# Optimization experiments

Measured on AMD Instinct MI355X. Metric: run time of the kernel, lower is better.

Reference implementation:

```python
import jax, jax.numpy as jnp
import numpy as np


def setup_inputs() -> dict:
    key = jax.random.key(0)
    k1, k2, k3 = jax.random.split(key, 3)
    H, W = 4096, 4096
    KH, KW = 3, 3
    return {
        "input": jax.random.normal(k1, (H, W), dtype=jnp.float32),
        "weight": jax.random.normal(k2, (KH, KW), dtype=jnp.float32),
        "bias": jax.random.normal(k3, (1,), dtype=jnp.float32),
    }


def reference(input, weight, bias):
    # VALID 2D cross-correlation of a single-channel image with a single kernel,
    # identical math to the original scalar double-loop: Y[i,j] = sum(X[i:i+h, j:j+w] * K) + b.
    x = input[None, None, :, :]   # NCHW, N=C=1
    k = weight[None, None, :, :]  # OIHW, O=I=1
    y = jax.lax.conv_general_dilated(
        x, k,
        window_strides=(1, 1),
        padding="VALID",
        dimension_numbers=("NCHW", "OIHW", "NCHW"),
    )[0, 0]  # [H-kh+1, W-kw+1]
    return y + bias[0]
```

## Files before the change

### kernel.cpp

```cpp
#include <hip/hip_runtime.h>

#define IW 4096
#define IH 4096
#define OH 4094
#define OW 4094
#define CG 1024
#define NWG 4096
#define XCHUNK 512

typedef float f32x4 __attribute__((ext_vector_type(4)));
typedef float f32x2 __attribute__((ext_vector_type(2)));

__global__ __launch_bounds__(256) void conv3x3_r4p(
    const float* __restrict__ in, const float* __restrict__ wgt,
    const float* __restrict__ bias, float* __restrict__ out) {

    int b   = blockIdx.x;
    int swz = (b & 7) * XCHUNK + (b >> 3);
    int idx = swz * 256 + (int)threadIdx.x;

    int cg   = idx & (CG - 1);
    int rg   = idx >> 10;
    int x    = cg << 2;
    int row0 = rg << 2;

    float wv[9];
#pragma unroll
    for (int i = 0; i < 9; ++i) wv[i] = wgt[i];
    float bs = bias[0];

    int nr    = (row0 + 4 <= OH) ? 4 : (OH - row0);
    int nload = nr + 2;

    float r[6][6];
#pragma unroll
    for (int t = 0; t < 6; ++t) {
        if (t < nload) {
            const float* rp = in + (size_t)(row0 + t) * IW + x;
            float4 a = *reinterpret_cast<const float4*>(rp);
            r[t][0] = a.x; r[t][1] = a.y; r[t][2] = a.z; r[t][3] = a.w;
            if (x + 5 < IW) {
                float2 e = *reinterpret_cast<const float2*>(rp + 4);
                r[t][4] = e.x; r[t][5] = e.y;
            } else { r[t][4] = 0.f; r[t][5] = 0.f; }
        } else {
#pragma unroll
            for (int j = 0; j < 6; ++j) r[t][j] = 0.f;
        }
    }

    float acc[4][4];
#pragma unroll
    for (int i = 0; i < 4; ++i)
#pragma unroll
        for (int c = 0; c < 4; ++c) acc[i][c] = bs;

#pragma unroll
    for (int orow = 0; orow < 4; ++orow) {
#pragma unroll
        for (int kh = 0; kh < 3; ++kh) {
            int t = orow + kh;
            float w0 = wv[kh * 3 + 0], w1 = wv[kh * 3 + 1], w2 = wv[kh * 3 + 2];
#pragma unroll
            for (int c = 0; c < 4; ++c)
                acc[orow][c] += w0 * r[t][c] + w1 * r[t][c + 1] + w2 * r[t][c + 2];
        }
    }

    int nc = (x + 4 <= OW) ? 4 : (OW - x);
#pragma unroll
    for (int orow = 0; orow < 4; ++orow) {
        if (orow < nr) {
            float* op = out + (size_t)(row0 + orow) * OW + x;
            if (nc == 4) {
                if ((orow & 1) == 0) {
                    *reinterpret_cast<f32x4*>(op) =
                        f32x4{ acc[orow][0], acc[orow][1], acc[orow][2], acc[orow][3] };
                } else {
                    *reinterpret_cast<f32x2*>(op)     = f32x2{ acc[orow][0], acc[orow][1] };
                    *reinterpret_cast<f32x2*>(op + 2) = f32x2{ acc[orow][2], acc[orow][3] };
                }
            } else {
                *reinterpret_cast<f32x2*>(op) = f32x2{ acc[orow][0], acc[orow][1] };
            }
        }
    }
}

extern "C" void kernel_launch(void* const* d_in, const int* in_sizes, int n_in,
                              void* d_out, int out_size, void* d_ws, size_t ws_size,
                              hipStream_t stream) {
    const float* in   = (const float*)d_in[0];
    const float* wgt  = (const float*)d_in[1];
    const float* bias = (const float*)d_in[2];
    float* out        = (float*)d_out;

    conv3x3_r4p<<<NWG, 256, 0, stream>>>(in, wgt, bias, out);
}
```

Before: 29.76 us.

## Compute two column tiles per thread and use nontemporal output stores

Result: slower. 30.96 us (+4.0%).

```diff
diff --git a/kernel.cpp b/kernel.cpp
--- a/kernel.cpp
+++ b/kernel.cpp
@@ -1,28 +1,30 @@
 #include <hip/hip_runtime.h>
 
 #define IW 4096
-#define IH 4096
 #define OH 4094
 #define OW 4094
-#define CG 1024
-#define NWG 4096
-#define XCHUNK 512
+#define NWG 2048
+#define XCHUNK 256
 
 typedef float f32x4 __attribute__((ext_vector_type(4)));
 typedef float f32x2 __attribute__((ext_vector_type(2)));
 
-__global__ __launch_bounds__(256) void conv3x3_r4p(
+__global__ __launch_bounds__(256) void conv3x3_dual(
     const float* __restrict__ in, const float* __restrict__ wgt,
     const float* __restrict__ bias, float* __restrict__ out) {
 
-    int b   = blockIdx.x;
-    int swz = (b & 7) * XCHUNK + (b >> 3);
-    int idx = swz * 256 + (int)threadIdx.x;
+    int b    = blockIdx.x;
+    int swz  = (b & 7) * XCHUNK + (b >> 3);
+    int lane = (int)threadIdx.x & 63;
+    int wib  = (int)threadIdx.x >> 6;
 
-    int cg   = idx & (CG - 1);
-    int rg   = idx >> 10;
-    int x    = cg << 2;
+    int wid  = swz * 4 + wib;
+    int wc   = wid & 7;
+    int rg   = wid >> 3;
     int row0 = rg << 2;
+
+    int x0 = wc * 512 + lane * 4;
+    int x1 = x0 + 256;
 
     float wv[9];
 #pragma unroll
@@ -32,56 +34,76 @@
     int nr    = (row0 + 4 <= OH) ? 4 : (OH - row0);
     int nload = nr + 2;
 
-    float r[6][6];
+    float r0[6][6], r1[6][6];
 #pragma unroll
     for (int t = 0; t < 6; ++t) {
         if (t < nload) {
-            const float* rp = in + (size_t)(row0 + t) * IW + x;
-            float4 a = *reinterpret_cast<const float4*>(rp);
-            r[t][0] = a.x; r[t][1] = a.y; r[t][2] = a.z; r[t][3] = a.w;
-            if (x + 5 < IW) {
-                float2 e = *reinterpret_cast<const float2*>(rp + 4);
-                r[t][4] = e.x; r[t][5] = e.y;
-            } else { r[t][4] = 0.f; r[t][5] = 0.f; }
+            const float* rp = in + (size_t)(row0 + t) * IW;
+            f32x4 a0 = *reinterpret_cast<const f32x4*>(rp + x0);
+            f32x4 a1 = *reinterpret_cast<const f32x4*>(rp + x1);
+            f32x2 e0 = *reinterpret_cast<const f32x2*>(rp + x0 + 4);
+            float e1a = 0.f, e1b = 0.f;
+            if (x1 + 5 < IW) {
+                f32x2 e1 = *reinterpret_cast<const f32x2*>(rp + x1 + 4);
+                e1a = e1[0]; e1b = e1[1];
+            }
+            r0[t][0]=a0[0]; r0[t][1]=a0[1]; r0[t][2]=a0[2]; r0[t][3]=a0[3];
+            r0[t][4]=e0[0]; r0[t][5]=e0[1];
+            r1[t][0]=a1[0]; r1[t][1]=a1[1]; r1[t][2]=a1[2]; r1[t][3]=a1[3];
+            r1[t][4]=e1a;   r1[t][5]=e1b;
         } else {
 #pragma unroll
-            for (int j = 0; j < 6; ++j) r[t][j] = 0.f;
+            for (int j = 0; j < 6; ++j) { r0[t][j] = 0.f; r1[t][j] = 0.f; }
         }
     }
 
-    float acc[4][4];
+    float acc0[4][4], acc1[4][4];
 #pragma unroll
     for (int i = 0; i < 4; ++i)
 #pragma unroll
-        for (int c = 0; c < 4; ++c) acc[i][c] = bs;
+        for (int c = 0; c < 4; ++c) { acc0[i][c] = bs; acc1[i][c] = bs; }
 
 #pragma unroll
     for (int orow = 0; orow < 4; ++orow) {
 #pragma unroll
         for (int kh = 0; kh < 3; ++kh) {
             int t = orow + kh;
-            float w0 = wv[kh * 3 + 0], w1 = wv[kh * 3 + 1], w2 = wv[kh * 3 + 2];
+            float w0 = wv[kh*3+0], w1 = wv[kh*3+1], w2 = wv[kh*3+2];
 #pragma unroll
-            for (int c = 0; c < 4; ++c)
-                acc[orow][c] += w0 * r[t][c] + w1 * r[t][c + 1] + w2 * r[t][c + 2];
+            for (int c = 0; c < 4; ++c) {
+                acc0[orow][c] += w0*r0[t][c] + w1*r0[t][c+1] + w2*r0[t][c+2];
+                acc1[orow][c] += w0*r1[t][c] + w1*r1[t][c+1] + w2*r1[t][c+2];
+            }
         }
     }
 
-    int nc = (x + 4 <= OW) ? 4 : (OW - x);
+    int nc1 = (x1 + 4 <= OW) ? 4 : (OW - x1);
 #pragma unroll
     for (int orow = 0; orow < 4; ++orow) {
         if (orow < nr) {
-            float* op = out + (size_t)(row0 + orow) * OW + x;
-            if (nc == 4) {
-                if ((orow & 1) == 0) {
-                    *reinterpret_cast<f32x4*>(op) =
-                        f32x4{ acc[orow][0], acc[orow][1], acc[orow][2], acc[orow][3] };
+            float* op0 = out + (size_t)(row0 + orow) * OW + x0;
+            float* op1 = out + (size_t)(row0 + orow) * OW + x1;
+            if ((orow & 1) == 0) {
+                f32x4 v = { acc0[orow][0], acc0[orow][1], acc0[orow][2], acc0[orow][3] };
+                __builtin_nontemporal_store(v, reinterpret_cast<f32x4*>(op0));
+                if (nc1 == 4) {
+                    f32x4 u = { acc1[orow][0], acc1[orow][1], acc1[orow][2], acc1[orow][3] };
+                    __builtin_nontemporal_store(u, reinterpret_cast<f32x4*>(op1));
                 } else {
-                    *reinterpret_cast<f32x2*>(op)     = f32x2{ acc[orow][0], acc[orow][1] };
-                    *reinterpret_cast<f32x2*>(op + 2) = f32x2{ acc[orow][2], acc[orow][3] };
+                    f32x2 u = { acc1[orow][0], acc1[orow][1] };
+                    __builtin_nontemporal_store(u, reinterpret_cast<f32x2*>(op1));
                 }
             } else {
-                *reinterpret_cast<f32x2*>(op) = f32x2{ acc[orow][0], acc[orow][1] };
+                f32x2 v0 = { acc0[orow][0], acc0[orow][1] };
+                f32x2 v1 = { acc0[orow][2], acc0[orow][3] };
+                __builtin_nontemporal_store(v0, reinterpret_cast<f32x2*>(op0));
+                __builtin_nontemporal_store(v1, reinterpret_cast<f32x2*>(op0 + 2));
+                f32x2 u0 = { acc1[orow][0], acc1[orow][1] };
+                __builtin_nontemporal_store(u0, reinterpret_cast<f32x2*>(op1));
+                if (nc1 == 4) {
+                    f32x2 u1 = { acc1[orow][2], acc1[orow][3] };
+                    __builtin_nontemporal_store(u1, reinterpret_cast<f32x2*>(op1 + 2));
+                }
             }
         }
     }
@@ -95,5 +117,5 @@
     const float* bias = (const float*)d_in[2];
     float* out        = (float*)d_out;
 
-    conv3x3_r4p<<<NWG, 256, 0, stream>>>(in, wgt, bias, out);
+    conv3x3_dual<<<NWG, 256, 0, stream>>>(in, wgt, bias, out);
 }
```
